# Performance work log

Measured on AMD Instinct MI355X. Metric: run time of the kernel, lower is better.

## Reference

```python
import jax, jax.numpy as jnp
import numpy as np

N_SRC, N_DST, N_EDGE, D = 100000, 40000, 600000, 128
LN_EPS = 1e-5

def _mlp(x, w1, b1, w2, b2, g, beta):
    # anemoi MLP: Linear -> SiLU -> Linear -> LayerNorm
    h = jax.nn.silu(x @ w1 + b1)
    h = h @ w2 + b2
    mu = jnp.mean(h, axis=-1, keepdims=True)
    var = jnp.var(h, axis=-1, keepdims=True)
    return (h - mu) * jax.lax.rsqrt(var + LN_EPS) * g + beta

def setup_inputs() -> dict:
    key = jax.random.key(0)
    ks = jax.random.split(key, 12)
    def rn(k, shape, scale):
        return jax.random.normal(k, shape, dtype=jnp.float32) * scale
    w_scale = 0.05
    return dict(
        x_src=rn(ks[0], (N_SRC, D), 1.0),
        x_dst=rn(ks[1], (N_DST, D), 1.0),
        edge_attr=rn(ks[2], (N_EDGE, D), 1.0),
        edge_index=jnp.stack([
            jax.random.randint(ks[3], (N_EDGE,), 0, N_SRC),
            jax.random.randint(ks[4], (N_EDGE,), 0, N_DST)]).astype(jnp.int32),
        edge_w1=rn(ks[5], (3 * D, D), w_scale), edge_b1=jnp.zeros((D,), jnp.float32),
        edge_w2=rn(ks[6], (D, D), w_scale), edge_b2=jnp.zeros((D,), jnp.float32),
        edge_g=jnp.ones((D,), jnp.float32), edge_beta=jnp.zeros((D,), jnp.float32),
        node_w1=rn(ks[7], (2 * D, D), w_scale), node_b1=jnp.zeros((D,), jnp.float32),
        node_w2=rn(ks[8], (D, D), w_scale), node_b2=jnp.zeros((D,), jnp.float32),
        node_g=jnp.ones((D,), jnp.float32), node_beta=jnp.zeros((D,), jnp.float32),
    )

def reference(x_src, x_dst, edge_attr, edge_index,
              edge_w1, edge_b1, edge_w2, edge_b2, edge_g, edge_beta,
              node_w1, node_b1, node_w2, node_b2, node_g, node_beta):
    src, dst = edge_index[0], edge_index[1]
    # GraphConv message: x_i = dst node feats, x_j = src node feats (PyG source_to_target)
    x_i = x_dst[dst]              # [E, D] gather
    x_j = x_src[src]              # [E, D] gather
    edges_new = _mlp(jnp.concatenate([x_i, x_j, edge_attr], axis=-1),
                     edge_w1, edge_b1, edge_w2, edge_b2, edge_g, edge_beta) + edge_attr
    # sum-aggregate messages to dst nodes (chunked sum == single sum)
    agg = jax.ops.segment_sum(edges_new, dst, num_segments=N_DST)  # [N_DST, D]
    nodes_new_dst = _mlp(jnp.concatenate([x_dst, agg], axis=-1),
                         node_w1, node_b1, node_w2, node_b2, node_g, node_beta) + x_dst
    # update_src_nodes=True branch
    nodes_new_src = _mlp(jnp.concatenate([x_src, x_src], axis=-1),
                         node_w1, node_b1, node_w2, node_b2, node_g, node_beta) + x_src
    return nodes_new_src, nodes_new_dst, edges_new
```

## Files before the change

kernel.cpp:

```cpp
#include <hip/hip_runtime.h>
#include <hip/hip_bf16.h>

#define NSRC  100000
#define NDST  40000
#define NEDGE 600000

#define GB_OFF     0ull
#define W1F_OFF    2048ull
#define W2F_OFF    (W1F_OFF + 98304ull)
#define NW1F_OFF   (W2F_OFF + 32768ull)
#define NW2F_OFF   (NW1F_OFF + 65536ull)
#define NW1SF_OFF  (NW2F_OFF + 32768ull)
#define DEG_OFF    (NW1SF_OFF + 32768ull)
#define CSR_OFF    (DEG_OFF + 160000ull)
#define CUR_OFF    (CSR_OFF + 160016ull)
#define CE_OFF     (CUR_OFF + 160000ull)
#define BSUM_OFF   (CE_OFF + 2400000ull)
#define AGG_OFF    (BSUM_OFF + 1024ull)
#define WS_REQUIRED (AGG_OFF + 10240000ull)

typedef __bf16 bf16;
typedef __attribute__((ext_vector_type(8))) __bf16 bf16x8;
typedef __attribute__((ext_vector_type(4))) float f32x4;

__device__ __forceinline__ unsigned short bfbits(float f) {
    return __builtin_bit_cast(unsigned short, (__bf16)f);
}

__device__ __forceinline__ f32x4 mfma16(bf16x8 a, bf16x8 b, f32x4 c) {
    return __builtin_amdgcn_mfma_f32_16x16x32_bf16(a, b, c, 0, 0, 0);
}

__device__ __forceinline__ bf16x8 pack8(float4 a, float4 b) {
    union { uint4 u; bf16x8 v; } o;
    o.u.x = (unsigned)bfbits(a.x) | ((unsigned)bfbits(a.y) << 16);
    o.u.y = (unsigned)bfbits(a.z) | ((unsigned)bfbits(a.w) << 16);
    o.u.z = (unsigned)bfbits(b.x) | ((unsigned)bfbits(b.y) << 16);
    o.u.w = (unsigned)bfbits(b.z) | ((unsigned)bfbits(b.w) << 16);
    return o.v;
}

__device__ __forceinline__ bf16x8 cvt8p(const float* p) {
    return pack8(*(const float4*)p, *(const float4*)(p + 4));
}

__device__ __forceinline__ void cas_add2(unsigned* p, float a0, float a1) {
    unsigned old = __hip_atomic_load(p, __ATOMIC_RELAXED, __HIP_MEMORY_SCOPE_AGENT);
    while (true) {
        float f0 = __builtin_bit_cast(float, (old & 0xffffu) << 16) + a0;
        float f1 = __builtin_bit_cast(float, old & 0xffff0000u) + a1;
        unsigned nv = (unsigned)bfbits(f0) | ((unsigned)bfbits(f1) << 16);
        unsigned prev = atomicCAS(p, old, nv);
        if (prev == old) break;
        old = prev;
    }
}

__global__ __launch_bounds__(256) void prep_kernel(
    const float* __restrict__ w1, const float* __restrict__ w2,
    const float* __restrict__ nw1, const float* __restrict__ nw2,
    bf16* __restrict__ w1f, bf16* __restrict__ w2f,
    bf16* __restrict__ nw1f, bf16* __restrict__ nw2f, bf16* __restrict__ nw1sf) {
    int i = blockIdx.x * 256 + threadIdx.x;
    if (i < 49152) {
        int j = i & 7, lane = (i >> 3) & 63, f = (i >> 9) & 3;
        int rest = i >> 11; int ks = rest % 12, wc = rest / 12;
        int k = ks * 32 + (lane >> 4) * 8 + j;
        int n = wc * 64 + f * 16 + (lane & 15);
        w1f[i] = (bf16)w1[k * 128 + n];
    } else if (i < 65536) {
        int q = i - 49152;
        int j = q & 7, lane = (q >> 3) & 63, f = (q >> 9) & 3;
        int rest = q >> 11; int ks = rest & 3, wc = rest >> 2;
        int k = ks * 32 + (lane >> 4) * 8 + j;
        int n = wc * 64 + f * 16 + (lane & 15);
        w2f[q] = (bf16)w2[k * 128 + n];
    } else if (i < 98304) {
        int q = i - 65536;
        int j = q & 7, lane = (q >> 3) & 63, f = (q >> 9) & 3;
        int rest = q >> 11; int ks = rest & 7, wc = rest >> 3;
        int k = ks * 32 + (lane >> 4) * 8 + j;
        int n = wc * 64 + f * 16 + (lane & 15);
        nw1f[q] = (bf16)nw1[k * 128 + n];
    } else if (i < 114688) {
        int q = i - 98304;
        int j = q & 7, lane = (q >> 3) & 63, f = (q >> 9) & 3;
        int rest = q >> 11; int ks = rest & 3, wc = rest >> 2;
        int k = ks * 32 + (lane >> 4) * 8 + j;
        int n = wc * 64 + f * 16 + (lane & 15);
        nw2f[q] = (bf16)nw2[k * 128 + n];
    } else {
        int q = i - 114688;
        int j = q & 7, lane = (q >> 3) & 63, f = (q >> 9) & 3;
        int rest = q >> 11; int ks = rest & 3, wc = rest >> 2;
        int k = ks * 32 + (lane >> 4) * 8 + j;
        int n = wc * 64 + f * 16 + (lane & 15);
        nw1sf[q] = (bf16)(nw1[k * 128 + n] + nw1[(k + 128) * 128 + n]);
    }
}

__global__ void select_gbeta(const float* __restrict__ a, const float* __restrict__ b,
                             float* __restrict__ g_out, float* __restrict__ beta_out) {
    int t = threadIdx.x;
    bool a_is_g = (a[0] == 1.0f);
    const float* g  = a_is_g ? a : b;
    const float* be = a_is_g ? b : a;
    g_out[t]    = g[t];
    beta_out[t] = be[t];
}

__global__ __launch_bounds__(256) void hist_kernel(const int* __restrict__ eidx,
                                                   int* __restrict__ deg) {
    int e = blockIdx.x * 256 + threadIdx.x;
    if (e < NEDGE) {
        int d = min(max(eidx[NEDGE + e], 0), NDST - 1);
        atomicAdd(&deg[d], 1);
    }
}

__global__ __launch_bounds__(256) void scan1_kernel(const int* __restrict__ deg,
                                                    int* __restrict__ bsum) {
    __shared__ int wsum[4];
    int i = blockIdx.x * 256 + threadIdx.x;
    int v = (i < NDST) ? deg[i] : 0;
#pragma unroll
    for (int m = 1; m < 64; m <<= 1) v += __shfl_xor(v, m, 64);
    if ((threadIdx.x & 63) == 0) wsum[threadIdx.x >> 6] = v;
    __syncthreads();
    if (threadIdx.x == 0) bsum[blockIdx.x] = wsum[0] + wsum[1] + wsum[2] + wsum[3];
}

__global__ __launch_bounds__(256) void scan2_kernel(int* __restrict__ bsum, int nb) {
    __shared__ int buf[256];
    int t = threadIdx.x;
    int v = (t < nb) ? bsum[t] : 0;
    buf[t] = v;
    __syncthreads();
    for (int off = 1; off < 256; off <<= 1) {
        int add = (t >= off) ? buf[t - off] : 0;
        __syncthreads();
        buf[t] += add;
        __syncthreads();
    }
    if (t < nb) bsum[t] = buf[t] - v;
}

__global__ __launch_bounds__(256) void scan3_kernel(const int* __restrict__ deg,
                                                    const int* __restrict__ bsum,
                                                    int* __restrict__ csr,
                                                    int* __restrict__ cur) {
    __shared__ int buf[256];
    int i = blockIdx.x * 256 + threadIdx.x;
    int t = threadIdx.x;
    int v = (i < NDST) ? deg[i] : 0;
    buf[t] = v;
    __syncthreads();
    for (int off = 1; off < 256; off <<= 1) {
        int add = (t >= off) ? buf[t - off] : 0;
        __syncthreads();
        buf[t] += add;
        __syncthreads();
    }
    if (i < NDST) {
        int excl = bsum[blockIdx.x] + buf[t] - v;
        csr[i] = excl;
        cur[i] = excl;
        if (i == NDST - 1) csr[NDST] = NEDGE;
    }
}

__global__ __launch_bounds__(256) void scatter_kernel(const int* __restrict__ eidx,
                                                      int* __restrict__ cur,
                                                      int* __restrict__ ce) {
    int e = blockIdx.x * 256 + threadIdx.x;
    if (e < NEDGE) {
        int d = min(max(eidx[NEDGE + e], 0), NDST - 1);
        int pos = atomicAdd(&cur[d], 1);
        ce[pos] = e;
    }
}

__device__ __forceinline__ void mlp_tail(
    f32x4 (&acc)[2][4], char* sH, float* redS, float* redQ,
    const bf16x8* w2v, const float* b1, const float* b2,
    const float* g, const float* be,
    int wr, int wc, int lr, int lg, int lane,
    float (&outv)[2][4][4])
{
    {
        float b1c[4];
#pragma unroll
        for (int fc = 0; fc < 4; ++fc) b1c[fc] = b1[wc * 64 + fc * 16 + lr];
#pragma unroll
        for (int fr = 0; fr < 2; ++fr)
#pragma unroll
            for (int fc = 0; fc < 4; ++fc)
#pragma unroll
                for (int rg = 0; rg < 4; ++rg) {
                    int row = wr * 32 + fr * 16 + lg * 4 + rg;
                    int col = wc * 64 + fc * 16 + lr;
                    float v = acc[fr][fc][rg] + b1c[fc];
                    v = v / (1.f + __expf(-v));
                    *(bf16*)(sH + ((row * 256 + col * 2) ^ ((row & 7) << 4))) = (bf16)v;
                }
    }
    __syncthreads();

#pragma unroll
    for (int i = 0; i < 2; ++i)
#pragma unroll
        for (int j = 0; j < 4; ++j) acc[i][j] = f32x4{0.f, 0.f, 0.f, 0.f};
#pragma unroll
    for (int ks = 0; ks < 4; ++ks) {
        bf16x8 a[2], b[4];
#pragma unroll
        for (int f = 0; f < 2; ++f) {
            int ra = wr * 32 + f * 16 + lr;
            a[f] = *(const bf16x8*)(sH + ((ra * 256 + ks * 64 + lg * 16) ^ ((ra & 7) << 4)));
        }
#pragma unroll
        for (int fc = 0; fc < 4; ++fc)
            b[fc] = w2v[((wc * 4 + ks) * 4 + fc) * 64 + lane];
#pragma unroll
        for (int i = 0; i < 2; ++i)
#pragma unroll
            for (int j = 0; j < 4; ++j)
                acc[i][j] = mfma16(a[i], b[j], acc[i][j]);
    }

    float b2c[4], gc[4], bc[4];
#pragma unroll
    for (int fc = 0; fc < 4; ++fc) {
        int col = wc * 64 + fc * 16 + lr;
        b2c[fc] = b2[col]; gc[fc] = g[col]; bc[fc] = be[col];
    }
#pragma unroll
    for (int fr = 0; fr < 2; ++fr)
#pragma unroll
        for (int rg = 0; rg < 4; ++rg) {
            float s = 0.f, sq = 0.f;
#pragma unroll
            for (int fc = 0; fc < 4; ++fc) {
                float v = acc[fr][fc][rg] + b2c[fc];
                acc[fr][fc][rg] = v;
                s += v; sq += v * v;
            }
#pragma unroll
            for (int m = 1; m < 16; m <<= 1) {
                s  += __shfl_xor(s, m, 64);
                sq += __shfl_xor(sq, m, 64);
            }
            if (lr == 0) {
                int row = wr * 32 + fr * 16 + lg * 4 + rg;
                redS[row * 2 + wc] = s;
                redQ[row * 2 + wc] = sq;
            }
        }
    __syncthreads();

#pragma unroll
    for (int fr = 0; fr < 2; ++fr)
#pragma unroll
        for (int rg = 0; rg < 4; ++rg) {
            int row = wr * 32 + fr * 16 + lg * 4 + rg;
            float s  = redS[row * 2] + redS[row * 2 + 1];
            float sq = redQ[row * 2] + redQ[row * 2 + 1];
            float mean = s * (1.f / 128.f);
            float var  = fmaxf(sq * (1.f / 128.f) - mean * mean, 0.f);
            float rstd = rsqrtf(var + 1e-5f);
#pragma unroll
            for (int fc = 0; fc < 4; ++fc)
                outv[fr][fc][rg] = (acc[fr][fc][rg] - mean) * rstd * gc[fc] + bc[fc];
        }
}

__global__ __launch_bounds__(256, 3) void edge_mfma_sorted(
    const float* __restrict__ xsrc, const float* __restrict__ xdst,
    const float* __restrict__ attr, const int* __restrict__ eidx,
    const int* __restrict__ ce,
    const bf16* __restrict__ w1f,  const bf16* __restrict__ w2f,
    const float* __restrict__ b1,  const float* __restrict__ b2,
    const float* __restrict__ g,   const float* __restrict__ be,
    float* __restrict__ oute, unsigned* __restrict__ aggw)
{
    __shared__ __align__(16) char sH[32768];
    __shared__ float redS[256], redQ[256];
    __shared__ int sE[128], sS[128], sD[128];

    const int t = threadIdx.x;
    const long e0 = (long)blockIdx.x * 128;
    if (t < 128) {
        long pos = e0 + t;
        if (pos < NEDGE) {
            int e = ce[pos];
            sE[t] = e;
            sS[t] = min(max(eidx[e], 0), NSRC - 1);
            sD[t] = min(max(eidx[NEDGE + e], 0), NDST - 1);
        } else {
            sE[t] = -1; sS[t] = 0; sD[t] = -1;
        }
    }
    __syncthreads();

    const int lane = t & 63, w = t >> 6;
    const int wr = w >> 1, wc = w & 1;
    const int lr = lane & 15, lg = lane >> 4;

    const float* xi[4]; const float* xj[4]; const float* at[4];
#pragma unroll
    for (int f = 0; f < 4; ++f) {
        int row = wr * 64 + f * 16 + lr;
        long em = max(sE[row], 0);
        xi[f] = xdst + (long)sD[row] * 128 * (sD[row] >= 0 ? 1 : 0);
        if (sD[row] < 0) xi[f] = xdst;
        xj[f] = xsrc + (long)sS[row] * 128;
        at[f] = attr + em * 128;
    }

    const bf16x8* w1v = (const bf16x8*)w1f;
    const bf16x8* w2v = (const bf16x8*)w2f;

    f32x4 acc[4][4];
#pragma unroll
    for (int i = 0; i < 4; ++i)
#pragma unroll
        for (int j = 0; j < 4; ++j) acc[i][j] = f32x4{0.f, 0.f, 0.f, 0.f};

#pragma unroll
    for (int ks = 0; ks < 12; ++ks) {
        int koff = (ks & 3) * 32 + lg * 8;
        bf16x8 a[4], b[4];
#pragma unroll
        for (int f = 0; f < 4; ++f) {
            const float* p = (ks < 4 ? xi[f] : ks < 8 ? xj[f] : at[f]) + koff;
            a[f] = cvt8p(p);
        }
#pragma unroll
        for (int fc = 0; fc < 4; ++fc)
            b[fc] = w1v[((wc * 12 + ks) * 4 + fc) * 64 + lane];
#pragma unroll
        for (int f = 0; f < 4; ++f)
#pragma unroll
            for (int j = 0; j < 4; ++j)
                acc[f][j] = mfma16(a[f], b[j], acc[f][j]);
    }

    {
        float b1c[4];
#pragma unroll
        for (int fc = 0; fc < 4; ++fc) b1c[fc] = b1[wc * 64 + fc * 16 + lr];
#pragma unroll
        for (int fr = 0; fr < 4; ++fr)
#pragma unroll
            for (int fc = 0; fc < 4; ++fc)
#pragma unroll
                for (int rg = 0; rg < 4; ++rg) {
                    int row = wr * 64 + fr * 16 + lg * 4 + rg;
                    int col = wc * 64 + fc * 16 + lr;
                    float v = acc[fr][fc][rg] + b1c[fc];
                    v = v / (1.f + __expf(-v));
                    *(bf16*)(sH + ((row * 256 + col * 2) ^ ((row & 7) << 4))) = (bf16)v;
                }
    }
    __syncthreads();

#pragma unroll
    for (int i = 0; i < 4; ++i)
#pragma unroll
        for (int j = 0; j < 4; ++j) acc[i][j] = f32x4{0.f, 0.f, 0.f, 0.f};
#pragma unroll
    for (int ks = 0; ks < 4; ++ks) {
        bf16x8 a[4], b[4];
#pragma unroll
        for (int f = 0; f < 4; ++f) {
            int ra = wr * 64 + f * 16 + lr;
            a[f] = *(const bf16x8*)(sH + ((ra * 256 + ks * 64 + lg * 16) ^ ((ra & 7) << 4)));
        }
#pragma unroll
        for (int fc = 0; fc < 4; ++fc)
            b[fc] = w2v[((wc * 4 + ks) * 4 + fc) * 64 + lane];
#pragma unroll
        for (int f = 0; f < 4; ++f)
#pragma unroll
            for (int j = 0; j < 4; ++j)
                acc[f][j] = mfma16(a[f], b[j], acc[f][j]);
    }

    float b2c[4], gc[4], bc[4];
#pragma unroll
    for (int fc = 0; fc < 4; ++fc) {
        int col = wc * 64 + fc * 16 + lr;
        b2c[fc] = b2[col]; gc[fc] = g[col]; bc[fc] = be[col];
    }
#pragma unroll
    for (int fr = 0; fr < 4; ++fr)
#pragma unroll
        for (int rg = 0; rg < 4; ++rg) {
            float s = 0.f, sq = 0.f;
#pragma unroll
            for (int fc = 0; fc < 4; ++fc) {
                float v = acc[fr][fc][rg] + b2c[fc];
                acc[fr][fc][rg] = v;
                s += v; sq += v * v;
            }
#pragma unroll
            for (int m = 1; m < 16; m <<= 1) {
                s  += __shfl_xor(s, m, 64);
                sq += __shfl_xor(sq, m, 64);
            }
            if (lr == 0) {
                int row = wr * 64 + fr * 16 + lg * 4 + rg;
                redS[row * 2 + wc] = s;
                redQ[row * 2 + wc] = sq;
            }
        }
    __syncthreads();

#pragma unroll
    for (int fr = 0; fr < 4; ++fr)
#pragma unroll
        for (int rg = 0; rg < 4; ++rg) {
            int row = wr * 64 + fr * 16 + lg * 4 + rg;
            float s  = redS[row * 2] + redS[row * 2 + 1];
            float sq = redQ[row * 2] + redQ[row * 2 + 1];
            float mean = s * (1.f / 128.f);
            float var  = fmaxf(sq * (1.f / 128.f) - mean * mean, 0.f);
            float rstd = rsqrtf(var + 1e-5f);
            int e = sE[row];
            long em = max(e, 0);
#pragma unroll
            for (int fc = 0; fc < 4; ++fc) {
                int col = wc * 64 + fc * 16 + lr;
                float v = (acc[fr][fc][rg] - mean) * rstd * gc[fc] + bc[fc];
                v += attr[em * 128 + col];
                if (e >= 0) oute[(long)e * 128 + col] = v;
                *(bf16*)(sH + ((row * 256 + col * 2) ^ ((row & 7) << 4))) = (bf16)v;
            }
        }
    __syncthreads();

    {
        int p = t & 63;
        int q0 = (t >> 6) * 32;
        int cur = sD[q0];
        float s0 = 0.f, s1 = 0.f;
        for (int r = q0; r < q0 + 32; ++r) {
            int d = sD[r];
            if (d != cur) {
                if (cur >= 0) cas_add2(aggw + (long)cur * 64 + p, s0, s1);
                cur = d; s0 = 0.f; s1 = 0.f;
            }
            unsigned u = *(const unsigned*)(sH + ((r * 256 + p * 4) ^ ((r & 7) << 4)));
            s0 += __builtin_bit_cast(float, (u & 0xffffu) << 16);
            s1 += __builtin_bit_cast(float, u & 0xffff0000u);
        }
        if (cur >= 0) cas_add2(aggw + (long)cur * 64 + p, s0, s1);
    }
}

__global__ __launch_bounds__(256, 4) void node_src_mfma(
    const float* __restrict__ xsrc,
    const bf16* __restrict__ nw1sf, const bf16* __restrict__ nw2f,
    const float* __restrict__ b1, const float* __restrict__ b2,
    const float* __restrict__ g,  const float* __restrict__ be,
    float* __restrict__ outp)
{
    __shared__ __align__(16) char sH[16384];
    __shared__ float redS[128], redQ[128];

    const int t = threadIdx.x;
    const long r0 = (long)blockIdx.x * 64;
    const int lane = t & 63, w = t >> 6;
    const int wr = w >> 1, wc = w & 1;
    const int lr = lane & 15, lg = lane >> 4;

    long gr0 = r0 + wr * 32 + lr;      if (gr0 >= NSRC) gr0 = NSRC - 1;
    long gr1 = r0 + wr * 32 + 16 + lr; if (gr1 >= NSRC) gr1 = NSRC - 1;
    const float* x0 = xsrc + gr0 * 128;
    const float* x1 = xsrc + gr1 * 128;

    const bf16x8* w1v = (const bf16x8*)nw1sf;
    const bf16x8* w2v = (const bf16x8*)nw2f;

    f32x4 acc[2][4];
#pragma unroll
    for (int i = 0; i < 2; ++i)
#pragma unroll
        for (int j = 0; j < 4; ++j) acc[i][j] = f32x4{0.f, 0.f, 0.f, 0.f};

#pragma unroll
    for (int ks = 0; ks < 4; ++ks) {
        int k0 = ks * 32 + lg * 8;
        bf16x8 a0 = cvt8p(x0 + k0);
        bf16x8 a1 = cvt8p(x1 + k0);
        bf16x8 b[4];
#pragma unroll
        for (int fc = 0; fc < 4; ++fc)
            b[fc] = w1v[((wc * 4 + ks) * 4 + fc) * 64 + lane];
#pragma unroll
        for (int j = 0; j < 4; ++j) {
            acc[0][j] = mfma16(a0, b[j], acc[0][j]);
            acc[1][j] = mfma16(a1, b[j], acc[1][j]);
        }
    }

    float outv[2][4][4];
    mlp_tail(acc, sH, redS, redQ, w2v, b1, b2, g, be, wr, wc, lr, lg, lane, outv);

#pragma unroll
    for (int fr = 0; fr < 2; ++fr)
#pragma unroll
        for (int rg = 0; rg < 4; ++rg) {
            int row = wr * 32 + fr * 16 + lg * 4 + rg;
            long gr = r0 + row;
            if (gr < NSRC) {
#pragma unroll
                for (int fc = 0; fc < 4; ++fc) {
                    int col = wc * 64 + fc * 16 + lr;
                    outp[gr * 128 + col] = outv[fr][fc][rg] + xsrc[gr * 128 + col];
                }
            }
        }
}

__global__ __launch_bounds__(256, 4) void node_dst_mfma(
    const float* __restrict__ xdst, const bf16* __restrict__ agg16,
    const bf16* __restrict__ nw1f, const bf16* __restrict__ nw2f,
    const float* __restrict__ b1, const float* __restrict__ b2,
    const float* __restrict__ g,  const float* __restrict__ be,
    float* __restrict__ outp)
{
    __shared__ __align__(16) char sH[16384];
    __shared__ float redS[128], redQ[128];

    const int t = threadIdx.x;
    const long r0 = (long)blockIdx.x * 64;
    const int lane = t & 63, w = t >> 6;
    const int wr = w >> 1, wc = w & 1;
    const int lr = lane & 15, lg = lane >> 4;

    long gr0 = r0 + wr * 32 + lr;
    long gr1 = gr0 + 16;
    const float* x0 = xdst + gr0 * 128;
    const float* x1 = xdst + gr1 * 128;
    const bf16* a0p = agg16 + gr0 * 128;
    const bf16* a1p = agg16 + gr1 * 128;

    const bf16x8* w1v = (const bf16x8*)nw1f;
    const bf16x8* w2v = (const bf16x8*)nw2f;

    f32x4 acc[2][4];
#pragma unroll
    for (int i = 0; i < 2; ++i)
#pragma unroll
        for (int j = 0; j < 4; ++j) acc[i][j] = f32x4{0.f, 0.f, 0.f, 0.f};

#pragma unroll
    for (int ks = 0; ks < 4; ++ks) {
        int k0 = ks * 32 + lg * 8;
        bf16x8 a0 = cvt8p(x0 + k0);
        bf16x8 a1 = cvt8p(x1 + k0);
        bf16x8 b[4];
#pragma unroll
        for (int fc = 0; fc < 4; ++fc)
            b[fc] = w1v[((wc * 8 + ks) * 4 + fc) * 64 + lane];
#pragma unroll
        for (int j = 0; j < 4; ++j) {
            acc[0][j] = mfma16(a0, b[j], acc[0][j]);
            acc[1][j] = mfma16(a1, b[j], acc[1][j]);
        }
    }
#pragma unroll
    for (int ks = 0; ks < 4; ++ks) {
        int k0 = ks * 32 + lg * 8;
        bf16x8 a0 = *(const bf16x8*)(a0p + k0);
        bf16x8 a1 = *(const bf16x8*)(a1p + k0);
        bf16x8 b[4];
#pragma unroll
        for (int fc = 0; fc < 4; ++fc)
            b[fc] = w1v[((wc * 8 + 4 + ks) * 4 + fc) * 64 + lane];
#pragma unroll
        for (int j = 0; j < 4; ++j) {
            acc[0][j] = mfma16(a0, b[j], acc[0][j]);
            acc[1][j] = mfma16(a1, b[j], acc[1][j]);
        }
    }

    float outv[2][4][4];
    mlp_tail(acc, sH, redS, redQ, w2v, b1, b2, g, be, wr, wc, lr, lg, lane, outv);

#pragma unroll
    for (int fr = 0; fr < 2; ++fr)
#pragma unroll
        for (int rg = 0; rg < 4; ++rg) {
            int row = wr * 32 + fr * 16 + lg * 4 + rg;
            long gr = r0 + row;
#pragma unroll
            for (int fc = 0; fc < 4; ++fc) {
                int col = wc * 64 + fc * 16 + lr;
                outp[gr * 128 + col] = outv[fr][fc][rg] + xdst[gr * 128 + col];
            }
        }
}

extern "C" void kernel_launch(void* const* d_in, const int* in_sizes, int n_in,
                              void* d_out, int out_size, void* d_ws, size_t ws_size,
                              hipStream_t stream) {
    if (ws_size < WS_REQUIRED) return;

    const float* xsrc = nullptr; const float* xdst = nullptr;
    const float* attr = nullptr; const int*   eidx = nullptr;
    const float* ew1  = nullptr; const float* nw1  = nullptr;
    const float* w2s[2] = {nullptr, nullptr}; int n16384 = 0;
    const float* v128[8] = {nullptr}; int n128 = 0;

    for (int i = 0; i < n_in; ++i) {
        switch (in_sizes[i]) {
            case 12800000: xsrc = (const float*)d_in[i]; break;
            case 5120000:  xdst = (const float*)d_in[i]; break;
            case 76800000: attr = (const float*)d_in[i]; break;
            case 1200000:  eidx = (const int*)d_in[i];   break;
            case 49152:    ew1  = (const float*)d_in[i]; break;
            case 32768:    nw1  = (const float*)d_in[i]; break;
            case 16384:    if (n16384 < 2) w2s[n16384++] = (const float*)d_in[i]; break;
            case 128:      if (n128 < 8)   v128[n128++]  = (const float*)d_in[i]; break;
            default: break;
        }
    }
    if (!xsrc || !xdst || !attr || !eidx || !ew1 || !nw1 || n16384 != 2 || n128 != 8)
        return;

    const float* ew2 = w2s[0];
    const float* nw2 = w2s[1];
    const float* eb1 = v128[0]; const float* eb2 = v128[1];
    const float* egA = v128[2]; const float* egB = v128[3];
    const float* nb1 = v128[4]; const float* nb2 = v128[5];
    const float* ngA = v128[6]; const float* ngB = v128[7];

    char* ws = (char*)d_ws;
    float* egv  = (float*)(ws + GB_OFF);
    float* ebv  = egv + 128;
    float* ngv  = ebv + 128;
    float* nbv  = ngv + 128;
    bf16* w1f   = (bf16*)(ws + W1F_OFF);
    bf16* w2f   = (bf16*)(ws + W2F_OFF);
    bf16* nw1f  = (bf16*)(ws + NW1F_OFF);
    bf16* nw2f  = (bf16*)(ws + NW2F_OFF);
    bf16* nw1sf = (bf16*)(ws + NW1SF_OFF);
    int*  deg   = (int*)(ws + DEG_OFF);
    int*  csr   = (int*)(ws + CSR_OFF);
    int*  cur   = (int*)(ws + CUR_OFF);
    int*  ce    = (int*)(ws + CE_OFF);
    int*  bsum  = (int*)(ws + BSUM_OFF);
    bf16* agg16 = (bf16*)(ws + AGG_OFF);

    float* out      = (float*)d_out;
    float* out_src  = out;
    float* out_dst  = out + (long)NSRC * 128;
    float* out_edge = out + (long)(NSRC + NDST) * 128;

    const int NB = (NDST + 255) / 256;

    hipMemsetAsync(deg, 0, (size_t)NDST * sizeof(int), stream);
    hipMemsetAsync(agg16, 0, 10240000ull, stream);
    select_gbeta<<<1, 128, 0, stream>>>(egA, egB, egv, ebv);
    select_gbeta<<<1, 128, 0, stream>>>(ngA, ngB, ngv, nbv);
    prep_kernel<<<512, 256, 0, stream>>>(ew1, ew2, nw1, nw2, w1f, w2f, nw1f, nw2f, nw1sf);

    hist_kernel<<<(NEDGE + 255) / 256, 256, 0, stream>>>(eidx, deg);
    scan1_kernel<<<NB, 256, 0, stream>>>(deg, bsum);
    scan2_kernel<<<1, 256, 0, stream>>>(bsum, NB);
    scan3_kernel<<<NB, 256, 0, stream>>>(deg, bsum, csr, cur);
    scatter_kernel<<<(NEDGE + 255) / 256, 256, 0, stream>>>(eidx, cur, ce);

    edge_mfma_sorted<<<(NEDGE + 127) / 128, 256, 0, stream>>>(
        xsrc, xdst, attr, eidx, ce, w1f, w2f, eb1, eb2, egv, ebv,
        out_edge, (unsigned*)agg16);
    node_src_mfma<<<(NSRC + 63) / 64, 256, 0, stream>>>(
        xsrc, nw1sf, nw2f, nb1, nb2, ngv, nbv, out_src);
    node_dst_mfma<<<NDST / 64, 256, 0, stream>>>(
        xdst, agg16, nw1f, nw2f, nb1, nb2, ngv, nbv, out_dst);
}
```

Baseline: 564.8 us.

## Precompute per-node first-layer projections and gather them in edge kernel

The first edge-MLP linear layer is split by linearity. The x_dst and x_src parts are computed once per node in a new pre_node_kernel, with results parked in the output buffers. The edge kernel then does MFMA only over edge_attr and adds the gathered per-node fp32 projections, which cuts edge matmul work by two thirds at the cost of gathering fp32 partial results. The block index is also swizzled across 8 groups to change scheduling locality. Numerics shift slightly because the node projections stay fp32 instead of being summed inside one accumulation.

```diff
diff --git a/kernel.cpp b/kernel.cpp
--- a/kernel.cpp
+++ b/kernel.cpp
@@ -180,6 +180,62 @@
     }
 }
 
+__global__ __launch_bounds__(256, 4) void pre_node_kernel(
+    const float* __restrict__ x, int n,
+    const bf16* __restrict__ w1f, int ksbase,
+    float* __restrict__ outp)
+{
+    const int t = threadIdx.x;
+    const long r0 = (long)blockIdx.x * 64;
+    const int lane = t & 63, w = t >> 6;
+    const int wr = w >> 1, wc = w & 1;
+    const int lr = lane & 15, lg = lane >> 4;
+
+    long gr0 = r0 + wr * 32 + lr;      if (gr0 >= n) gr0 = n - 1;
+    long gr1 = r0 + wr * 32 + 16 + lr; if (gr1 >= n) gr1 = n - 1;
+    const float* x0 = x + gr0 * 128;
+    const float* x1 = x + gr1 * 128;
+
+    const bf16x8* w1v = (const bf16x8*)w1f;
+
+    f32x4 acc[2][4];
+#pragma unroll
+    for (int i = 0; i < 2; ++i)
+#pragma unroll
+        for (int j = 0; j < 4; ++j) acc[i][j] = f32x4{0.f, 0.f, 0.f, 0.f};
+
+#pragma unroll
+    for (int ks = 0; ks < 4; ++ks) {
+        int k0 = ks * 32 + lg * 8;
+        bf16x8 a0 = cvt8p(x0 + k0);
+        bf16x8 a1 = cvt8p(x1 + k0);
+        bf16x8 b[4];
+#pragma unroll
+        for (int fc = 0; fc < 4; ++fc)
+            b[fc] = w1v[((wc * 12 + ksbase + ks) * 4 + fc) * 64 + lane];
+#pragma unroll
+        for (int j = 0; j < 4; ++j) {
+            acc[0][j] = mfma16(a0, b[j], acc[0][j]);
+            acc[1][j] = mfma16(a1, b[j], acc[1][j]);
+        }
+    }
+
+#pragma unroll
+    for (int fr = 0; fr < 2; ++fr)
+#pragma unroll
+        for (int rg = 0; rg < 4; ++rg) {
+            int row = wr * 32 + fr * 16 + lg * 4 + rg;
+            long gr = r0 + row;
+            if (gr < n) {
+#pragma unroll
+                for (int fc = 0; fc < 4; ++fc) {
+                    int col = wc * 64 + fc * 16 + lr;
+                    outp[gr * 128 + col] = acc[fr][fc][rg];
+                }
+            }
+        }
+}
+
 __device__ __forceinline__ void mlp_tail(
     f32x4 (&acc)[2][4], char* sH, float* redS, float* redQ,
     const bf16x8* w2v, const float* b1, const float* b2,
@@ -275,9 +331,9 @@
 }
 
 __global__ __launch_bounds__(256, 3) void edge_mfma_sorted(
-    const float* __restrict__ xsrc, const float* __restrict__ xdst,
     const float* __restrict__ attr, const int* __restrict__ eidx,
     const int* __restrict__ ce,
+    const float* __restrict__ Pd,  const float* __restrict__ Ps,
     const bf16* __restrict__ w1f,  const bf16* __restrict__ w2f,
     const float* __restrict__ b1,  const float* __restrict__ b2,
     const float* __restrict__ g,   const float* __restrict__ be,
@@ -288,7 +344,8 @@
     __shared__ int sE[128], sS[128], sD[128];
 
     const int t = threadIdx.x;
-    const long e0 = (long)blockIdx.x * 128;
+    const int lb = (blockIdx.x & 7) * 586 + (blockIdx.x >> 3);
+    const long e0 = (long)lb * 128;
     if (t < 128) {
         long pos = e0 + t;
         if (pos < NEDGE) {
@@ -306,14 +363,11 @@
     const int wr = w >> 1, wc = w & 1;
     const int lr = lane & 15, lg = lane >> 4;
 
-    const float* xi[4]; const float* xj[4]; const float* at[4];
+    const float* at[4];
 #pragma unroll
     for (int f = 0; f < 4; ++f) {
         int row = wr * 64 + f * 16 + lr;
         long em = max(sE[row], 0);
-        xi[f] = xdst + (long)sD[row] * 128 * (sD[row] >= 0 ? 1 : 0);
-        if (sD[row] < 0) xi[f] = xdst;
-        xj[f] = xsrc + (long)sS[row] * 128;
         at[f] = attr + em * 128;
     }
 
@@ -327,23 +381,35 @@
         for (int j = 0; j < 4; ++j) acc[i][j] = f32x4{0.f, 0.f, 0.f, 0.f};
 
 #pragma unroll
-    for (int ks = 0; ks < 12; ++ks) {
-        int koff = (ks & 3) * 32 + lg * 8;
+    for (int ks = 0; ks < 4; ++ks) {
+        int koff = ks * 32 + lg * 8;
         bf16x8 a[4], b[4];
 #pragma unroll
-        for (int f = 0; f < 4; ++f) {
-            const float* p = (ks < 4 ? xi[f] : ks < 8 ? xj[f] : at[f]) + koff;
-            a[f] = cvt8p(p);
-        }
+        for (int f = 0; f < 4; ++f)
+            a[f] = cvt8p(at[f] + koff);
 #pragma unroll
         for (int fc = 0; fc < 4; ++fc)
-            b[fc] = w1v[((wc * 12 + ks) * 4 + fc) * 64 + lane];
+            b[fc] = w1v[((wc * 12 + 8 + ks) * 4 + fc) * 64 + lane];
 #pragma unroll
         for (int f = 0; f < 4; ++f)
 #pragma unroll
             for (int j = 0; j < 4; ++j)
                 acc[f][j] = mfma16(a[f], b[j], acc[f][j]);
     }
+
+#pragma unroll
+    for (int fr = 0; fr < 4; ++fr)
+#pragma unroll
+        for (int rg = 0; rg < 4; ++rg) {
+            int row = wr * 64 + fr * 16 + lg * 4 + rg;
+            const float* pd = Pd + (long)max(sD[row], 0) * 128;
+            const float* ps = Ps + (long)sS[row] * 128;
+#pragma unroll
+            for (int fc = 0; fc < 4; ++fc) {
+                int col = wc * 64 + fc * 16 + lr;
+                acc[fr][fc][rg] += pd[col] + ps[col];
+            }
+        }
 
     {
         float b1c[4];
@@ -673,8 +739,11 @@
     scan3_kernel<<<NB, 256, 0, stream>>>(deg, bsum, csr, cur);
     scatter_kernel<<<(NEDGE + 255) / 256, 256, 0, stream>>>(eidx, cur, ce);
 
+    pre_node_kernel<<<(NDST + 63) / 64, 256, 0, stream>>>(xdst, NDST, w1f, 0, out_dst);
+    pre_node_kernel<<<(NSRC + 63) / 64, 256, 0, stream>>>(xsrc, NSRC, w1f, 4, out_src);
+
     edge_mfma_sorted<<<(NEDGE + 127) / 128, 256, 0, stream>>>(
-        xsrc, xdst, attr, eidx, ce, w1f, w2f, eb1, eb2, egv, ebv,
+        attr, eidx, ce, out_dst, out_src, w1f, w2f, eb1, eb2, egv, ebv,
         out_edge, (unsigned*)agg16);
     node_src_mfma<<<(NSRC + 63) / 64, 256, 0, stream>>>(
         xsrc, nw1sf, nw2f, nb1, nb2, ngv, nbv, out_src);
```

Result: faster. 545.5 us (-3.4%).
